# Optimization experiments

Hardware: AMD Instinct MI355X
Metric: run time of the kernel (lower is better)

## Reference

```python
import jax, jax.numpy as jnp
import numpy as np

N = 100000   # nodes
E = 1600000  # edges
H = 2        # heads
F = 64       # out_feats per head
D = 256      # node feature dim
DE = 8       # edge feature dim
NEG_SLOPE = 0.2


def setup_inputs() -> dict:
    key = jax.random.key(0)
    ks = jax.random.split(key, 12)
    s = 0.05
    return {
        "feat_src": jax.random.normal(ks[0], (N, D), jnp.float32),
        "feat_edge": jax.random.normal(ks[1], (E, DE), jnp.float32),
        "edge_src": jax.random.randint(ks[2], (E,), 0, N, jnp.int32),
        "edge_dst": jax.random.randint(ks[3], (E,), 0, N, jnp.int32),
        "W_src": jax.random.normal(ks[4], (H * F, D), jnp.float32) * s,
        "W_dst": jax.random.normal(ks[5], (H * F, D), jnp.float32) * s,
        "b_dst": jax.random.normal(ks[6], (H * F,), jnp.float32) * s,
        "W_attn_src": jax.random.normal(ks[7], (H, D), jnp.float32) * s,
        "W_attn_dst": jax.random.normal(ks[8], (H, D), jnp.float32) * s,
        "W_attn_edge": jax.random.normal(ks[9], (H, DE), jnp.float32) * s,
        "W_ngnn": jax.random.normal(ks[10], (H * F, H * F), jnp.float32) * s,
        "b_ngnn": jax.random.normal(ks[11], (H * F,), jnp.float32) * s,
    }


def reference(feat_src, feat_edge, edge_src, edge_dst,
              W_src, W_dst, b_dst, W_attn_src, W_attn_dst, W_attn_edge,
              W_ngnn, b_ngnn):
    # node projections (graph is not a block -> feat_dst = feat_src)
    h_src = (feat_src @ W_src.T).reshape(N, H, F)          # [N,H,F]
    h_dst = (feat_src @ W_dst.T + b_dst).reshape(N, H, F)  # residual branch

    # per-node attention logits [N,H]
    a_src = feat_src @ W_attn_src.T
    a_dst = feat_src @ W_attn_dst.T
    a_edge = feat_edge @ W_attn_edge.T                     # [E,H]

    # per-edge score: u_add_v + edge term, LeakyReLU
    e = a_src[edge_src] + a_dst[edge_dst] + a_edge         # [E,H]
    e = jnp.where(e >= 0, e, NEG_SLOPE * e)

    # edge softmax over incoming edges of each destination node
    m = jax.ops.segment_max(e, edge_dst, num_segments=N)   # [N,H]
    ex = jnp.exp(e - m[edge_dst])
    z = jax.ops.segment_sum(ex, edge_dst, num_segments=N)  # [N,H]
    a = ex / z[edge_dst]                                   # [E,H]

    # weighted gather-scatter aggregation: u_mul_e -> sum per dst
    msg = h_src[edge_src] * a[:, :, None]                  # [E,H,F]
    rst = jax.ops.segment_sum(msg, edge_dst, num_segments=N)  # [N,H,F]

    # ngnn layer + ReLU
    rst = rst.reshape(N, H * F)
    rst = jax.nn.relu(rst @ W_ngnn.T + b_ngnn)
    rst = rst.reshape(N, H, F)

    # residual connection via dst_fc
    rst = rst + h_dst
    return rst
```

## Files before the change

kernel.cpp:

```cpp
#include <hip/hip_runtime.h>
#include <hip/hip_bf16.h>
#include <math.h>

#define NN 100000
#define EE 1600000
#define DD 256
#define DEE 8
#define HF 128
#define NEG_SLOPE 0.2f
#define NBUCK 196
#define P1_EPB 4096

typedef __bf16 bf16x8 __attribute__((ext_vector_type(8)));
typedef float  f32x4  __attribute__((ext_vector_type(4)));

__device__ inline ushort f2bf(float f) {
    uint32_t x = __builtin_bit_cast(uint32_t, f);
    x += 0x7fffu + ((x >> 16) & 1u);
    return (ushort)(x >> 16);
}
__device__ inline float bf2f(ushort u) {
    uint32_t x = ((uint32_t)u) << 16;
    return __builtin_bit_cast(float, x);
}
__device__ inline float u2f(uint u) { return __builtin_bit_cast(float, u); }
__device__ inline uint f2u(float f) { return __builtin_bit_cast(uint, f); }

__device__ inline void load_lds16(const void* g, void* l) {
    __builtin_amdgcn_global_load_lds(
        (const __attribute__((address_space(1))) void*)g,
        (__attribute__((address_space(3))) void*)l, 16, 0, 0);
}

__global__ __launch_bounds__(256) void f2bf_kernel(
    const float* __restrict__ in, ushort* __restrict__ out, int n)
{
    int i = (blockIdx.x * 256 + threadIdx.x) * 4;
    if (i + 3 < n) {
        float4 v = *(const float4*)(in + i);
        ushort4 o;
        o.x = f2bf(v.x); o.y = f2bf(v.y); o.z = f2bf(v.z); o.w = f2bf(v.w);
        *(ushort4*)(out + i) = o;
    } else {
        for (int c = 0; c < 4 && i + c < n; ++c) out[i + c] = f2bf(in[i + c]);
    }
}

template<int K, int MODE>
__global__ __launch_bounds__(256) void mfma_gemm(
    const ushort* __restrict__ Wb,
    const ushort* __restrict__ Xb,
    const float*  __restrict__ bias,
    const ushort* __restrict__ resid,
    void* __restrict__ outp)
{
    __shared__ ushort As[128 * 32];
    __shared__ ushort Bs[128 * 32];

    const int tid  = threadIdx.x;
    const int lane = tid & 63, wv = tid >> 6;
    const int wm = wv >> 1, wn = wv & 1;
    const int r = lane & 15, quad = lane >> 4;
    const int m0 = blockIdx.x * 128;

    f32x4 acc[4][4] = {};

    for (int k0 = 0; k0 < K; k0 += 32) {
#pragma unroll
        for (int t = 0; t < 2; ++t) {
            int is  = wv + t * 4;
            int row = is * 16 + (lane >> 2);
            int ko  = k0 + (lane & 3) * 8;
            load_lds16(Wb + (size_t)row * K + ko, &As[is * 512]);
            int gm = m0 + row; gm = gm < NN ? gm : NN - 1;
            load_lds16(Xb + (size_t)gm * K + ko, &Bs[is * 512]);
        }
        __syncthreads();
        bf16x8 a[4], b[4];
#pragma unroll
        for (int i = 0; i < 4; ++i) {
            a[i] = __builtin_bit_cast(bf16x8,
                   *(const f32x4*)&As[(wm * 64 + i * 16 + r) * 32 + quad * 8]);
            b[i] = __builtin_bit_cast(bf16x8,
                   *(const f32x4*)&Bs[(wn * 64 + i * 16 + r) * 32 + quad * 8]);
        }
#pragma unroll
        for (int i = 0; i < 4; ++i)
#pragma unroll
            for (int j = 0; j < 4; ++j)
                acc[i][j] = __builtin_amdgcn_mfma_f32_16x16x32_bf16(
                    a[i], b[j], acc[i][j], 0, 0, 0);
        __syncthreads();
    }

#pragma unroll
    for (int i = 0; i < 4; ++i) {
        int fbase = wm * 64 + i * 16 + quad * 4;
        float4 bv = make_float4(0.f, 0.f, 0.f, 0.f);
        if (MODE >= 1) bv = *(const float4*)(bias + fbase);
#pragma unroll
        for (int j = 0; j < 4; ++j) {
            int node = m0 + wn * 64 + j * 16 + r;
            if (node >= NN) continue;
            f32x4 v = acc[i][j];
            if (MODE >= 1) { v[0] += bv.x; v[1] += bv.y; v[2] += bv.z; v[3] += bv.w; }
            if (MODE == 2) {
                ushort4 rs = *(const ushort4*)(resid + (size_t)node * HF + fbase);
                float4 o;
                o.x = fmaxf(v[0], 0.f) + bf2f(rs.x);
                o.y = fmaxf(v[1], 0.f) + bf2f(rs.y);
                o.z = fmaxf(v[2], 0.f) + bf2f(rs.z);
                o.w = fmaxf(v[3], 0.f) + bf2f(rs.w);
                *(float4*)((float*)outp + (size_t)node * HF + fbase) = o;
            } else {
                ushort4 o;
                o.x = f2bf(v[0]); o.y = f2bf(v[1]); o.z = f2bf(v[2]); o.w = f2bf(v[3]);
                *(ushort4*)((ushort*)outp + (size_t)node * HF + fbase) = o;
            }
        }
    }
}

__global__ __launch_bounds__(256) void attn_logits_kernel(
    const float* __restrict__ feat,
    const float* __restrict__ Was, const float* __restrict__ Wad,
    float* __restrict__ a_src, float* __restrict__ a_dst,
    ushort* __restrict__ feat_bf)
{
    int wave = threadIdx.x >> 6, lane = threadIdx.x & 63;
    int node = blockIdx.x * 4 + wave;
    if (node >= NN) return;
    float4 f = *(const float4*)(feat + (size_t)node * DD + lane * 4);
    ushort4 fb;
    fb.x = f2bf(f.x); fb.y = f2bf(f.y); fb.z = f2bf(f.z); fb.w = f2bf(f.w);
    *(ushort4*)(feat_bf + (size_t)node * DD + lane * 4) = fb;

    float4 w0 = *(const float4*)(Was + 0 * DD + lane * 4);
    float4 w1 = *(const float4*)(Was + 1 * DD + lane * 4);
    float4 w2 = *(const float4*)(Wad + 0 * DD + lane * 4);
    float4 w3 = *(const float4*)(Wad + 1 * DD + lane * 4);
    float p0 = f.x * w0.x + f.y * w0.y + f.z * w0.z + f.w * w0.w;
    float p1 = f.x * w1.x + f.y * w1.y + f.z * w1.z + f.w * w1.w;
    float p2 = f.x * w2.x + f.y * w2.y + f.z * w2.z + f.w * w2.w;
    float p3 = f.x * w3.x + f.y * w3.y + f.z * w3.z + f.w * w3.w;
#pragma unroll
    for (int o = 32; o > 0; o >>= 1) {
        p0 += __shfl_xor(p0, o);
        p1 += __shfl_xor(p1, o);
        p2 += __shfl_xor(p2, o);
        p3 += __shfl_xor(p3, o);
    }
    if (lane == 0) {
        a_src[node * 2 + 0] = p0; a_src[node * 2 + 1] = p1;
        a_dst[node * 2 + 0] = p2; a_dst[node * 2 + 1] = p3;
    }
}

__global__ __launch_bounds__(256) void hist_kernel(
    const int* __restrict__ edge_dst, int* __restrict__ deg)
{
    int i = blockIdx.x * 256 + threadIdx.x;
    if (i < EE) atomicAdd(&deg[edge_dst[i]], 1);
}

#define SCAN_ELEMS 1024
__global__ __launch_bounds__(256) void scan1_kernel(
    const int* __restrict__ deg, int* __restrict__ offsets, int* __restrict__ blockSums)
{
    __shared__ int sd[256];
    int tid = threadIdx.x;
    int base = blockIdx.x * SCAN_ELEMS + tid * 4;
    int v[4];
#pragma unroll
    for (int c = 0; c < 4; ++c) v[c] = (base + c < NN) ? deg[base + c] : 0;
    int tsum = v[0] + v[1] + v[2] + v[3];
    sd[tid] = tsum;
    __syncthreads();
    for (int o = 1; o < 256; o <<= 1) {
        int x = (tid >= o) ? sd[tid - o] : 0;
        __syncthreads();
        sd[tid] += x;
        __syncthreads();
    }
    int excl = sd[tid] - tsum;
    int run = excl;
#pragma unroll
    for (int c = 0; c < 4; ++c) {
        if (base + c < NN) offsets[base + c] = run;
        run += v[c];
    }
    if (tid == 255) blockSums[blockIdx.x] = sd[255];
}

__global__ __launch_bounds__(128) void scan2_kernel(int* __restrict__ blockSums, int nb)
{
    __shared__ int sd[128];
    int tid = threadIdx.x;
    int tv = (tid < nb) ? blockSums[tid] : 0;
    sd[tid] = tv;
    __syncthreads();
    for (int o = 1; o < 128; o <<= 1) {
        int x = (tid >= o) ? sd[tid - o] : 0;
        __syncthreads();
        sd[tid] += x;
        __syncthreads();
    }
    if (tid < nb) blockSums[tid] = sd[tid] - tv;
}

__global__ __launch_bounds__(256) void scan3_kernel(
    int* __restrict__ offsets, const int* __restrict__ blockSums)
{
    int tid = threadIdx.x;
    int base = blockIdx.x * SCAN_ELEMS + tid * 4;
    int add = blockSums[blockIdx.x];
#pragma unroll
    for (int c = 0; c < 4; ++c)
        if (base + c < NN) offsets[base + c] += add;
    if (blockIdx.x == 0 && tid == 0) offsets[NN] = EE;
}

__global__ __launch_bounds__(256) void binit_kernel(
    const int* __restrict__ offsets, int* __restrict__ bcur)
{
    int t = threadIdx.x;
    if (t < NBUCK) bcur[t] = offsets[t * 512];
}

__global__ __launch_bounds__(256) void bucket_scatter_kernel(
    const int* __restrict__ edge_src, const int* __restrict__ edge_dst,
    const float* __restrict__ feat_edge,
    const float* __restrict__ a_src, const float* __restrict__ a_dst,
    const float* __restrict__ Wae,
    int* __restrict__ bcur, uint4* __restrict__ staging)
{
    __shared__ int cnt[256];
    __shared__ int basearr[256];
    __shared__ int run[256];
    const int tid = threadIdx.x;
    const int b0 = blockIdx.x * P1_EPB;

    cnt[tid] = 0;
    __syncthreads();
#pragma unroll
    for (int j = 0; j < P1_EPB / 256; ++j) {
        int i = b0 + j * 256 + tid;
        if (i < EE) atomicAdd(&cnt[edge_dst[i] >> 9], 1);
    }
    __syncthreads();
    if (tid < NBUCK) {
        int c = cnt[tid];
        basearr[tid] = c ? atomicAdd(&bcur[tid], c) : 0;
    }
    run[tid] = 0;
    __syncthreads();

    float4 w00 = ((const float4*)Wae)[0], w01 = ((const float4*)Wae)[1];
    float4 w10 = ((const float4*)Wae)[2], w11 = ((const float4*)Wae)[3];

#pragma unroll
    for (int j = 0; j < P1_EPB / 256; ++j) {
        int i = b0 + j * 256 + tid;
        if (i >= EE) continue;
        int s = edge_src[i], d = edge_dst[i];
        float4 e0 = ((const float4*)feat_edge)[i * 2 + 0];
        float4 e1 = ((const float4*)feat_edge)[i * 2 + 1];
        float ae0 = e0.x*w00.x + e0.y*w00.y + e0.z*w00.z + e0.w*w00.w
                  + e1.x*w01.x + e1.y*w01.y + e1.z*w01.z + e1.w*w01.w;
        float ae1 = e0.x*w10.x + e0.y*w10.y + e0.z*w10.z + e0.w*w10.w
                  + e1.x*w11.x + e1.y*w11.y + e1.z*w11.z + e1.w*w11.w;
        float v0 = a_src[s * 2 + 0] + a_dst[d * 2 + 0] + ae0;
        float v1 = a_src[s * 2 + 1] + a_dst[d * 2 + 1] + ae1;
        v0 = (v0 >= 0.f) ? v0 : NEG_SLOPE * v0;
        v1 = (v1 >= 0.f) ? v1 : NEG_SLOPE * v1;
        int bk = d >> 9;
        int ofs = atomicAdd(&run[bk], 1);
        staging[basearr[bk] + ofs] = make_uint4((uint)s, (uint)d, f2u(v0), f2u(v1));
    }
}

__global__ __launch_bounds__(256) void fine_scatter_kernel(
    const int* __restrict__ offsets,
    const uint4* __restrict__ staging, uint4* __restrict__ pairs)
{
    __shared__ int cur[512];
    const int tid = threadIdx.x;
    const int nb0 = blockIdx.x * 512;
    const int ncnt = (NN - nb0 < 512) ? (NN - nb0) : 512;
    for (int i = tid; i < ncnt; i += 256) cur[i] = offsets[nb0 + i];
    __syncthreads();
    const int lo = offsets[nb0];
    const int hi = offsets[nb0 + ncnt];
    for (int j = lo + tid; j < hi; j += 256) {
        uint4 it = staging[j];
        int n = (int)it.y - nb0;
        int pos = atomicAdd(&cur[n], 1);
        pairs[pos] = it;
    }
}

__global__ __launch_bounds__(256) void aggregate_fused(
    const int* __restrict__ offsets,
    const uint4* __restrict__ pairs,
    const ushort* __restrict__ hsrc,
    ushort* __restrict__ agg)
{
    int wave = threadIdx.x >> 6, lane = threadIdx.x & 63;
    int node = blockIdx.x * 4 + wave;
    if (node >= NN) return;
    int off = offsets[node], end = offsets[node + 1];
    int n = end - off;
    uint* aggw = (uint*)agg;
    if (n <= 0) { aggw[(size_t)node * 64 + lane] = 0; return; }
    const uint* h2 = (const uint*)hsrc;
    int hh = lane >> 5;

    float acc0a = 0.f, acc1a = 0.f, acc0b = 0.f, acc1b = 0.f;
    float zi0, zi1;

    if (n <= 64) {
        uint4 pr = (lane < n) ? pairs[off + lane]
                              : make_uint4(0u, 0u, 0xff800000u, 0xff800000u);
        float s0 = u2f(pr.z), s1 = u2f(pr.w);
        float m0 = s0, m1 = s1;
#pragma unroll
        for (int o = 32; o > 0; o >>= 1) {
            m0 = fmaxf(m0, __shfl_xor(m0, o));
            m1 = fmaxf(m1, __shfl_xor(m1, o));
        }
        float ex0 = (lane < n) ? __expf(s0 - m0) : 0.f;
        float ex1 = (lane < n) ? __expf(s1 - m1) : 0.f;
        float z0 = ex0, z1 = ex1;
#pragma unroll
        for (int o = 32; o > 0; o >>= 1) {
            z0 += __shfl_xor(z0, o);
            z1 += __shfl_xor(z1, o);
        }
        zi0 = 1.f / z0; zi1 = 1.f / z1;
        int srcu = (int)pr.x;
        int k = 0;
        for (; k + 1 < n; k += 2) {
            int   sA = __shfl(srcu, k),     sB = __shfl(srcu, k + 1);
            float eA0 = __shfl(ex0, k),     eB0 = __shfl(ex0, k + 1);
            float eA1 = __shfl(ex1, k),     eB1 = __shfl(ex1, k + 1);
            uint pA = h2[(size_t)sA * 64 + lane];
            uint pB = h2[(size_t)sB * 64 + lane];
            float wA = hh ? eA1 : eA0;
            float wB = hh ? eB1 : eB0;
            acc0a = fmaf(wA, bf2f((ushort)(pA & 0xffff)), acc0a);
            acc1a = fmaf(wA, bf2f((ushort)(pA >> 16)),    acc1a);
            acc0b = fmaf(wB, bf2f((ushort)(pB & 0xffff)), acc0b);
            acc1b = fmaf(wB, bf2f((ushort)(pB >> 16)),    acc1b);
        }
        if (k < n) {
            int   sA = __shfl(srcu, k);
            float eA0 = __shfl(ex0, k), eA1 = __shfl(ex1, k);
            uint pA = h2[(size_t)sA * 64 + lane];
            float wA = hh ? eA1 : eA0;
            acc0a = fmaf(wA, bf2f((ushort)(pA & 0xffff)), acc0a);
            acc1a = fmaf(wA, bf2f((ushort)(pA >> 16)),    acc1a);
        }
    } else {
        float m0 = -INFINITY, m1 = -INFINITY;
        for (int c0 = 0; c0 < n; c0 += 64) {
            if (c0 + lane < n) {
                uint4 pr = pairs[off + c0 + lane];
                m0 = fmaxf(m0, u2f(pr.z));
                m1 = fmaxf(m1, u2f(pr.w));
            }
        }
#pragma unroll
        for (int o = 32; o > 0; o >>= 1) {
            m0 = fmaxf(m0, __shfl_xor(m0, o));
            m1 = fmaxf(m1, __shfl_xor(m1, o));
        }
        float z0 = 0.f, z1 = 0.f;
        for (int c0 = 0; c0 < n; c0 += 64) {
            if (c0 + lane < n) {
                uint4 pr = pairs[off + c0 + lane];
                z0 += __expf(u2f(pr.z) - m0);
                z1 += __expf(u2f(pr.w) - m1);
            }
        }
#pragma unroll
        for (int o = 32; o > 0; o >>= 1) {
            z0 += __shfl_xor(z0, o);
            z1 += __shfl_xor(z1, o);
        }
        zi0 = 1.f / z0; zi1 = 1.f / z1;
        for (int c0 = 0; c0 < n; c0 += 64) {
            int cn = n - c0; if (cn > 64) cn = 64;
            uint4 pr = (lane < cn) ? pairs[off + c0 + lane]
                                   : make_uint4(0u, 0u, 0u, 0u);
            float ex0 = (lane < cn) ? __expf(u2f(pr.z) - m0) : 0.f;
            float ex1 = (lane < cn) ? __expf(u2f(pr.w) - m1) : 0.f;
            int srcu = (int)pr.x;
            for (int k = 0; k < cn; ++k) {
                int   sA = __shfl(srcu, k);
                float eA0 = __shfl(ex0, k), eA1 = __shfl(ex1, k);
                uint pA = h2[(size_t)sA * 64 + lane];
                float wA = hh ? eA1 : eA0;
                acc0a = fmaf(wA, bf2f((ushort)(pA & 0xffff)), acc0a);
                acc1a = fmaf(wA, bf2f((ushort)(pA >> 16)),    acc1a);
            }
        }
    }

    float zi = hh ? zi1 : zi0;
    float r0 = (acc0a + acc0b) * zi;
    float r1 = (acc1a + acc1b) * zi;
    aggw[(size_t)node * 64 + lane] = ((uint)f2bf(r1) << 16) | (uint)f2bf(r0);
}

extern "C" void kernel_launch(void* const* d_in, const int* in_sizes, int n_in,
                              void* d_out, int out_size, void* d_ws, size_t ws_size,
                              hipStream_t stream) {
    (void)in_sizes; (void)n_in; (void)out_size; (void)ws_size;
    const float* feat_src  = (const float*)d_in[0];
    const float* feat_edge = (const float*)d_in[1];
    const int*   edge_src  = (const int*)d_in[2];
    const int*   edge_dst  = (const int*)d_in[3];
    const float* W_src     = (const float*)d_in[4];
    const float* W_dst     = (const float*)d_in[5];
    const float* b_dst     = (const float*)d_in[6];
    const float* W_attn_src  = (const float*)d_in[7];
    const float* W_attn_dst  = (const float*)d_in[8];
    const float* W_attn_edge = (const float*)d_in[9];
    const float* W_ngnn    = (const float*)d_in[10];
    const float* b_ngnn    = (const float*)d_in[11];
    float* out = (float*)d_out;

    char* base = (char*)d_ws;
    size_t off = 0;
    auto take = [&](size_t bytes) -> void* {
        void* p = base + off;
        off = (off + bytes + 511) & ~(size_t)511;
        return p;
    };
    ushort* feat_bf  = (ushort*)take((size_t)NN * DD * 2);
    ushort* h_src_bf = (ushort*)take((size_t)NN * HF * 2);
    uint4*  staging  = (uint4*)take((size_t)EE * 16);
    uint4*  pairs    = (uint4*)take((size_t)EE * 16);
    float*  a_src_b  = (float*)take((size_t)NN * 2 * 4);
    float*  a_dst_b  = (float*)take((size_t)NN * 2 * 4);
    int*    deg      = (int*)take((size_t)NN * 4);
    int*    offsets  = (int*)take((size_t)(NN + 1) * 4);
    int*    bcur     = (int*)take((size_t)NBUCK * 4);
    int*    blockSums= (int*)take(512);
    ushort* Wsrc_bf  = (ushort*)take((size_t)HF * DD * 2);
    ushort* Wdst_bf  = (ushort*)take((size_t)HF * DD * 2);
    ushort* Wngnn_bf = (ushort*)take((size_t)HF * HF * 2);
    ushort* h_dst_bf = (ushort*)staging;
    ushort* agg_bf   = feat_bf;

    const int NB_SCAN = (NN + SCAN_ELEMS - 1) / SCAN_ELEMS;
    const int GB_E  = (EE + 255) / 256;
    const int GB_M  = (NN + 127) / 128;
    const int GB_N4 = (NN + 3) / 4;
    const int GB_P1 = (EE + P1_EPB - 1) / P1_EPB;

    hipMemsetAsync(deg, 0, (size_t)NN * 4, stream);
    hipLaunchKernelGGL(hist_kernel, dim3(GB_E), dim3(256), 0, stream, edge_dst, deg);
    hipLaunchKernelGGL(scan1_kernel, dim3(NB_SCAN), dim3(256), 0, stream, deg, offsets, blockSums);
    hipLaunchKernelGGL(scan2_kernel, dim3(1), dim3(128), 0, stream, blockSums, NB_SCAN);
    hipLaunchKernelGGL(scan3_kernel, dim3(NB_SCAN), dim3(256), 0, stream, offsets, blockSums);
    hipLaunchKernelGGL(binit_kernel, dim3(1), dim3(256), 0, stream, offsets, bcur);

    hipLaunchKernelGGL(attn_logits_kernel, dim3(GB_N4), dim3(256), 0, stream,
                       feat_src, W_attn_src, W_attn_dst, a_src_b, a_dst_b, feat_bf);

    hipLaunchKernelGGL(f2bf_kernel, dim3((HF * DD / 4 + 255) / 256), dim3(256), 0, stream,
                       W_src, Wsrc_bf, HF * DD);
    hipLaunchKernelGGL(f2bf_kernel, dim3((HF * DD / 4 + 255) / 256), dim3(256), 0, stream,
                       W_dst, Wdst_bf, HF * DD);
    hipLaunchKernelGGL(f2bf_kernel, dim3((HF * HF / 4 + 255) / 256), dim3(256), 0, stream,
                       W_ngnn, Wngnn_bf, HF * HF);

    hipLaunchKernelGGL(bucket_scatter_kernel, dim3(GB_P1), dim3(256), 0, stream,
                       edge_src, edge_dst, feat_edge, a_src_b, a_dst_b, W_attn_edge,
                       bcur, staging);
    hipLaunchKernelGGL(fine_scatter_kernel, dim3(NBUCK), dim3(256), 0, stream,
                       offsets, staging, pairs);

    hipLaunchKernelGGL((mfma_gemm<DD, 0>), dim3(GB_M), dim3(256), 0, stream,
                       Wsrc_bf, feat_bf, (const float*)nullptr, (const ushort*)nullptr, h_src_bf);
    hipLaunchKernelGGL((mfma_gemm<DD, 1>), dim3(GB_M), dim3(256), 0, stream,
                       Wdst_bf, feat_bf, b_dst, (const ushort*)nullptr, h_dst_bf);

    hipLaunchKernelGGL(aggregate_fused, dim3(GB_N4), dim3(256), 0, stream,
                       offsets, pairs, h_src_bf, agg_bf);

    hipLaunchKernelGGL((mfma_gemm<HF, 2>), dim3(GB_M), dim3(256), 0, stream,
                       Wngnn_bf, agg_bf, b_ngnn, h_dst_bf, out);
}
```

Measured before the change: 550.8 us.

## Fuse src/dst projection GEMMs, merge weight casts, single-pass softmax aggregation

Combines the two node-projection GEMMs into one dual-output kernel that loads each feature tile once, merges the three weight conversion launches into one, and folds the bucket-cursor init into the scan kernel. The aggregation kernel now accumulates the softmax denominator in the same pass as the weighted sum, using an LDS stash instead of shuffles, which removes an extra read of the edge pairs for high-degree nodes. It also shrinks the bucket-scatter block size. Launch count and redundant feature reads go down, at the cost of a smaller node tile in the dual GEMM and more LDS traffic in aggregation.

Result: faster. 521.4 us (-5.3%).

```diff
diff --git a/kernel.cpp b/kernel.cpp
--- a/kernel.cpp
+++ b/kernel.cpp
@@ -9,7 +9,7 @@
 #define HF 128
 #define NEG_SLOPE 0.2f
 #define NBUCK 196
-#define P1_EPB 4096
+#define P1_EPB 1024
 
 typedef __bf16 bf16x8 __attribute__((ext_vector_type(8)));
 typedef float  f32x4  __attribute__((ext_vector_type(4)));
@@ -25,6 +25,8 @@
 }
 __device__ inline float u2f(uint u) { return __builtin_bit_cast(float, u); }
 __device__ inline uint f2u(float f) { return __builtin_bit_cast(uint, f); }
+__device__ inline float lo_bf(uint p) { return __builtin_bit_cast(float, p << 16); }
+__device__ inline float hi_bf(uint p) { return __builtin_bit_cast(float, p & 0xffff0000u); }
 
 __device__ inline void load_lds16(const void* g, void* l) {
     __builtin_amdgcn_global_load_lds(
@@ -32,27 +34,112 @@
         (__attribute__((address_space(3))) void*)l, 16, 0, 0);
 }
 
-__global__ __launch_bounds__(256) void f2bf_kernel(
-    const float* __restrict__ in, ushort* __restrict__ out, int n)
+__global__ __launch_bounds__(256) void f2bf3_kernel(
+    const float* __restrict__ wa, const float* __restrict__ wb,
+    const float* __restrict__ wc,
+    ushort* __restrict__ oa, ushort* __restrict__ ob, ushort* __restrict__ oc)
 {
     int i = (blockIdx.x * 256 + threadIdx.x) * 4;
-    if (i + 3 < n) {
-        float4 v = *(const float4*)(in + i);
-        ushort4 o;
-        o.x = f2bf(v.x); o.y = f2bf(v.y); o.z = f2bf(v.z); o.w = f2bf(v.w);
-        *(ushort4*)(out + i) = o;
-    } else {
-        for (int c = 0; c < 4 && i + c < n; ++c) out[i + c] = f2bf(in[i + c]);
-    }
-}
-
-template<int K, int MODE>
-__global__ __launch_bounds__(256) void mfma_gemm(
+    const int na = HF * DD, nb2 = 2 * HF * DD, nc3 = 2 * HF * DD + HF * HF;
+    const float* src; ushort* dst; int o;
+    if (i < na)       { src = wa; dst = oa; o = i; }
+    else if (i < nb2) { src = wb; dst = ob; o = i - na; }
+    else if (i < nc3) { src = wc; dst = oc; o = i - nb2; }
+    else return;
+    float4 v = *(const float4*)(src + o);
+    ushort4 u;
+    u.x = f2bf(v.x); u.y = f2bf(v.y); u.z = f2bf(v.z); u.w = f2bf(v.w);
+    *(ushort4*)(dst + o) = u;
+}
+
+template<int K>
+__global__ __launch_bounds__(256) void mfma_gemm_dual(
+    const ushort* __restrict__ W0,
+    const ushort* __restrict__ W1,
+    const ushort* __restrict__ Xb,
+    const float*  __restrict__ bias1,
+    ushort* __restrict__ out0, ushort* __restrict__ out1)
+{
+    __shared__ ushort As[2][128 * 32];
+    __shared__ ushort Bs[64 * 32];
+
+    const int tid  = threadIdx.x;
+    const int lane = tid & 63, wv = tid >> 6;
+    const int wm = wv >> 1, wn = wv & 1;
+    const int r = lane & 15, quad = lane >> 4;
+    const int m0 = blockIdx.x * 64;
+
+    f32x4 acc[2][4][2] = {};
+
+    for (int k0 = 0; k0 < K; k0 += 32) {
+#pragma unroll
+        for (int t = 0; t < 2; ++t) {
+            int is  = wv + t * 4;
+            int row = is * 16 + (lane >> 2);
+            int ko  = k0 + (lane & 3) * 8;
+            load_lds16(W0 + (size_t)row * K + ko, &As[0][is * 512]);
+            load_lds16(W1 + (size_t)row * K + ko, &As[1][is * 512]);
+        }
+        {
+            int is  = wv;
+            int row = is * 16 + (lane >> 2);
+            int ko  = k0 + (lane & 3) * 8;
+            int gm = m0 + row; gm = gm < NN ? gm : NN - 1;
+            load_lds16(Xb + (size_t)gm * K + ko, &Bs[is * 512]);
+        }
+        __syncthreads();
+        bf16x8 a[2][4], b[2];
+#pragma unroll
+        for (int i = 0; i < 4; ++i) {
+            a[0][i] = __builtin_bit_cast(bf16x8,
+                      *(const f32x4*)&As[0][(wm * 64 + i * 16 + r) * 32 + quad * 8]);
+            a[1][i] = __builtin_bit_cast(bf16x8,
+                      *(const f32x4*)&As[1][(wm * 64 + i * 16 + r) * 32 + quad * 8]);
+        }
+#pragma unroll
+        for (int j = 0; j < 2; ++j)
+            b[j] = __builtin_bit_cast(bf16x8,
+                   *(const f32x4*)&Bs[(wn * 32 + j * 16 + r) * 32 + quad * 8]);
+#pragma unroll
+        for (int s = 0; s < 2; ++s)
+#pragma unroll
+            for (int i = 0; i < 4; ++i)
+#pragma unroll
+                for (int j = 0; j < 2; ++j)
+                    acc[s][i][j] = __builtin_amdgcn_mfma_f32_16x16x32_bf16(
+                        a[s][i], b[j], acc[s][i][j], 0, 0, 0);
+        __syncthreads();
+    }
+
+#pragma unroll
+    for (int s = 0; s < 2; ++s) {
+        ushort* outp = s ? out1 : out0;
+#pragma unroll
+        for (int i = 0; i < 4; ++i) {
+            int fbase = wm * 64 + i * 16 + quad * 4;
+            float4 bv = make_float4(0.f, 0.f, 0.f, 0.f);
+            if (s == 1) bv = *(const float4*)(bias1 + fbase);
+#pragma unroll
+            for (int j = 0; j < 2; ++j) {
+                int node = m0 + wn * 32 + j * 16 + r;
+                if (node >= NN) continue;
+                f32x4 v = acc[s][i][j];
+                v[0] += bv.x; v[1] += bv.y; v[2] += bv.z; v[3] += bv.w;
+                ushort4 o;
+                o.x = f2bf(v[0]); o.y = f2bf(v[1]); o.z = f2bf(v[2]); o.w = f2bf(v[3]);
+                *(ushort4*)(outp + (size_t)node * HF + fbase) = o;
+            }
+        }
+    }
+}
+
+template<int K>
+__global__ __launch_bounds__(256) void mfma_gemm_ngnn(
     const ushort* __restrict__ Wb,
     const ushort* __restrict__ Xb,
     const float*  __restrict__ bias,
     const ushort* __restrict__ resid,
-    void* __restrict__ outp)
+    float* __restrict__ outp)
 {
     __shared__ ushort As[128 * 32];
     __shared__ ushort Bs[128 * 32];
@@ -96,27 +183,19 @@
 #pragma unroll
     for (int i = 0; i < 4; ++i) {
         int fbase = wm * 64 + i * 16 + quad * 4;
-        float4 bv = make_float4(0.f, 0.f, 0.f, 0.f);
-        if (MODE >= 1) bv = *(const float4*)(bias + fbase);
+        float4 bv = *(const float4*)(bias + fbase);
 #pragma unroll
         for (int j = 0; j < 4; ++j) {
             int node = m0 + wn * 64 + j * 16 + r;
             if (node >= NN) continue;
             f32x4 v = acc[i][j];
-            if (MODE >= 1) { v[0] += bv.x; v[1] += bv.y; v[2] += bv.z; v[3] += bv.w; }
-            if (MODE == 2) {
-                ushort4 rs = *(const ushort4*)(resid + (size_t)node * HF + fbase);
-                float4 o;
-                o.x = fmaxf(v[0], 0.f) + bf2f(rs.x);
-                o.y = fmaxf(v[1], 0.f) + bf2f(rs.y);
-                o.z = fmaxf(v[2], 0.f) + bf2f(rs.z);
-                o.w = fmaxf(v[3], 0.f) + bf2f(rs.w);
-                *(float4*)((float*)outp + (size_t)node * HF + fbase) = o;
-            } else {
-                ushort4 o;
-                o.x = f2bf(v[0]); o.y = f2bf(v[1]); o.z = f2bf(v[2]); o.w = f2bf(v[3]);
-                *(ushort4*)((ushort*)outp + (size_t)node * HF + fbase) = o;
-            }
+            ushort4 rs = *(const ushort4*)(resid + (size_t)node * HF + fbase);
+            float4 o;
+            o.x = fmaxf(v[0] + bv.x, 0.f) + bf2f(rs.x);
+            o.y = fmaxf(v[1] + bv.y, 0.f) + bf2f(rs.y);
+            o.z = fmaxf(v[2] + bv.z, 0.f) + bf2f(rs.z);
+            o.w = fmaxf(v[3] + bv.w, 0.f) + bf2f(rs.w);
+            *(float4*)(outp + (size_t)node * HF + fbase) = o;
         }
     }
 }
@@ -209,22 +288,22 @@
 }
 
 __global__ __launch_bounds__(256) void scan3_kernel(
-    int* __restrict__ offsets, const int* __restrict__ blockSums)
+    int* __restrict__ offsets, const int* __restrict__ blockSums,
+    int* __restrict__ bcur)
 {
     int tid = threadIdx.x;
     int base = blockIdx.x * SCAN_ELEMS + tid * 4;
     int add = blockSums[blockIdx.x];
 #pragma unroll
-    for (int c = 0; c < 4; ++c)
-        if (base + c < NN) offsets[base + c] += add;
+    for (int c = 0; c < 4; ++c) {
+        int idx = base + c;
+        if (idx < NN) {
+            int v = offsets[idx] + add;
+            offsets[idx] = v;
+            if ((idx & 511) == 0) bcur[idx >> 9] = v;
+        }
+    }
     if (blockIdx.x == 0 && tid == 0) offsets[NN] = EE;
-}
-
-__global__ __launch_bounds__(256) void binit_kernel(
-    const int* __restrict__ offsets, int* __restrict__ bcur)
-{
-    int t = threadIdx.x;
-    if (t < NBUCK) bcur[t] = offsets[t * 512];
 }
 
 __global__ __launch_bounds__(256) void bucket_scatter_kernel(
@@ -305,6 +384,7 @@
     const ushort* __restrict__ hsrc,
     ushort* __restrict__ agg)
 {
+    __shared__ uint4 stash[4][64];
     int wave = threadIdx.x >> 6, lane = threadIdx.x & 63;
     int node = blockIdx.x * 4 + wave;
     if (node >= NN) return;
@@ -315,50 +395,29 @@
     const uint* h2 = (const uint*)hsrc;
     int hh = lane >> 5;
 
-    float acc0a = 0.f, acc1a = 0.f, acc0b = 0.f, acc1b = 0.f;
-    float zi0, zi1;
+    float acc0 = 0.f, acc1 = 0.f, z0 = 0.f, z1 = 0.f;
 
     if (n <= 64) {
         uint4 pr = (lane < n) ? pairs[off + lane]
                               : make_uint4(0u, 0u, 0xff800000u, 0xff800000u);
-        float s0 = u2f(pr.z), s1 = u2f(pr.w);
-        float m0 = s0, m1 = s1;
+        float m0 = u2f(pr.z), m1 = u2f(pr.w);
 #pragma unroll
         for (int o = 32; o > 0; o >>= 1) {
             m0 = fmaxf(m0, __shfl_xor(m0, o));
             m1 = fmaxf(m1, __shfl_xor(m1, o));
         }
-        float ex0 = (lane < n) ? __expf(s0 - m0) : 0.f;
-        float ex1 = (lane < n) ? __expf(s1 - m1) : 0.f;
-        float z0 = ex0, z1 = ex1;
-#pragma unroll
-        for (int o = 32; o > 0; o >>= 1) {
-            z0 += __shfl_xor(z0, o);
-            z1 += __shfl_xor(z1, o);
-        }
-        zi0 = 1.f / z0; zi1 = 1.f / z1;
-        int srcu = (int)pr.x;
-        int k = 0;
-        for (; k + 1 < n; k += 2) {
-            int   sA = __shfl(srcu, k),     sB = __shfl(srcu, k + 1);
-            float eA0 = __shfl(ex0, k),     eB0 = __shfl(ex0, k + 1);
-            float eA1 = __shfl(ex1, k),     eB1 = __shfl(ex1, k + 1);
-            uint pA = h2[(size_t)sA * 64 + lane];
-            uint pB = h2[(size_t)sB * 64 + lane];
-            float wA = hh ? eA1 : eA0;
-            float wB = hh ? eB1 : eB0;
-            acc0a = fmaf(wA, bf2f((ushort)(pA & 0xffff)), acc0a);
-            acc1a = fmaf(wA, bf2f((ushort)(pA >> 16)),    acc1a);
-            acc0b = fmaf(wB, bf2f((ushort)(pB & 0xffff)), acc0b);
-            acc1b = fmaf(wB, bf2f((ushort)(pB >> 16)),    acc1b);
-        }
-        if (k < n) {
-            int   sA = __shfl(srcu, k);
-            float eA0 = __shfl(ex0, k), eA1 = __shfl(ex1, k);
-            uint pA = h2[(size_t)sA * 64 + lane];
-            float wA = hh ? eA1 : eA0;
-            acc0a = fmaf(wA, bf2f((ushort)(pA & 0xffff)), acc0a);
-            acc1a = fmaf(wA, bf2f((ushort)(pA >> 16)),    acc1a);
+        float ex0 = (lane < n) ? __expf(u2f(pr.z) - m0) : 0.f;
+        float ex1 = (lane < n) ? __expf(u2f(pr.w) - m1) : 0.f;
+        z0 = ex0; z1 = ex1;
+        stash[wave][lane] = make_uint4(pr.x, f2u(ex0), f2u(ex1), 0u);
+        __builtin_amdgcn_wave_barrier();
+#pragma unroll 4
+        for (int k = 0; k < n; ++k) {
+            uint4 st = stash[wave][k];
+            uint p = h2[(size_t)st.x * 64 + lane];
+            float w = hh ? u2f(st.z) : u2f(st.y);
+            acc0 = fmaf(w, lo_bf(p), acc0);
+            acc1 = fmaf(w, hi_bf(p), acc1);
         }
     } else {
         float m0 = -INFINITY, m1 = -INFINITY;
@@ -374,41 +433,39 @@
             m0 = fmaxf(m0, __shfl_xor(m0, o));
             m1 = fmaxf(m1, __shfl_xor(m1, o));
         }
-        float z0 = 0.f, z1 = 0.f;
-        for (int c0 = 0; c0 < n; c0 += 64) {
-            if (c0 + lane < n) {
-                uint4 pr = pairs[off + c0 + lane];
-                z0 += __expf(u2f(pr.z) - m0);
-                z1 += __expf(u2f(pr.w) - m1);
-            }
-        }
-#pragma unroll
-        for (int o = 32; o > 0; o >>= 1) {
-            z0 += __shfl_xor(z0, o);
-            z1 += __shfl_xor(z1, o);
-        }
-        zi0 = 1.f / z0; zi1 = 1.f / z1;
         for (int c0 = 0; c0 < n; c0 += 64) {
             int cn = n - c0; if (cn > 64) cn = 64;
-            uint4 pr = (lane < cn) ? pairs[off + c0 + lane]
-                                   : make_uint4(0u, 0u, 0u, 0u);
-            float ex0 = (lane < cn) ? __expf(u2f(pr.z) - m0) : 0.f;
-            float ex1 = (lane < cn) ? __expf(u2f(pr.w) - m1) : 0.f;
-            int srcu = (int)pr.x;
+            uint srcv = 0; float ex0 = 0.f, ex1 = 0.f;
+            if (lane < cn) {
+                uint4 pr = pairs[off + c0 + lane];
+                srcv = pr.x;
+                ex0 = __expf(u2f(pr.z) - m0);
+                ex1 = __expf(u2f(pr.w) - m1);
+                z0 += ex0; z1 += ex1;
+            }
+            stash[wave][lane] = make_uint4(srcv, f2u(ex0), f2u(ex1), 0u);
+            __builtin_amdgcn_wave_barrier();
+#pragma unroll 4
             for (int k = 0; k < cn; ++k) {
-                int   sA = __shfl(srcu, k);
-                float eA0 = __shfl(ex0, k), eA1 = __shfl(ex1, k);
-                uint pA = h2[(size_t)sA * 64 + lane];
-                float wA = hh ? eA1 : eA0;
-                acc0a = fmaf(wA, bf2f((ushort)(pA & 0xffff)), acc0a);
-                acc1a = fmaf(wA, bf2f((ushort)(pA >> 16)),    acc1a);
+                uint4 st = stash[wave][k];
+                uint p = h2[(size_t)st.x * 64 + lane];
+                float w = hh ? u2f(st.z) : u2f(st.y);
+                acc0 = fmaf(w, lo_bf(p), acc0);
+                acc1 = fmaf(w, hi_bf(p), acc1);
             }
-        }
-    }
-
-    float zi = hh ? zi1 : zi0;
-    float r0 = (acc0a + acc0b) * zi;
-    float r1 = (acc1a + acc1b) * zi;
+            __builtin_amdgcn_wave_barrier();
+        }
+    }
+
+#pragma unroll
+    for (int o = 32; o > 0; o >>= 1) {
+        z0 += __shfl_xor(z0, o);
+        z1 += __shfl_xor(z1, o);
+    }
+    float zi = hh ? ((z1 > 0.f) ? 1.f / z1 : 0.f)
+                  : ((z0 > 0.f) ? 1.f / z0 : 0.f);
+    float r0 = acc0 * zi;
+    float r1 = acc1 * zi;
     aggw[(size_t)node * 64 + lane] = ((uint)f2bf(r1) << 16) | (uint)f2bf(r0);
 }
 
@@ -456,25 +513,23 @@
     const int NB_SCAN = (NN + SCAN_ELEMS - 1) / SCAN_ELEMS;
     const int GB_E  = (EE + 255) / 256;
     const int GB_M  = (NN + 127) / 128;
+    const int GB_M64= (NN + 63) / 64;
     const int GB_N4 = (NN + 3) / 4;
     const int GB_P1 = (EE + P1_EPB - 1) / P1_EPB;
+    const int W3_N  = (2 * HF * DD + HF * HF) / 4;
+    const int GB_W3 = (W3_N + 255) / 256;
 
     hipMemsetAsync(deg, 0, (size_t)NN * 4, stream);
     hipLaunchKernelGGL(hist_kernel, dim3(GB_E), dim3(256), 0, stream, edge_dst, deg);
     hipLaunchKernelGGL(scan1_kernel, dim3(NB_SCAN), dim3(256), 0, stream, deg, offsets, blockSums);
     hipLaunchKernelGGL(scan2_kernel, dim3(1), dim3(128), 0, stream, blockSums, NB_SCAN);
-    hipLaunchKernelGGL(scan3_kernel, dim3(NB_SCAN), dim3(256), 0, stream, offsets, blockSums);
-    hipLaunchKernelGGL(binit_kernel, dim3(1), dim3(256), 0, stream, offsets, bcur);
+    hipLaunchKernelGGL(scan3_kernel, dim3(NB_SCAN), dim3(256), 0, stream, offsets, blockSums, bcur);
 
     hipLaunchKernelGGL(attn_logits_kernel, dim3(GB_N4), dim3(256), 0, stream,
                        feat_src, W_attn_src, W_attn_dst, a_src_b, a_dst_b, feat_bf);
 
-    hipLaunchKernelGGL(f2bf_kernel, dim3((HF * DD / 4 + 255) / 256), dim3(256), 0, stream,
-                       W_src, Wsrc_bf, HF * DD);
-    hipLaunchKernelGGL(f2bf_kernel, dim3((HF * DD / 4 + 255) / 256), dim3(256), 0, stream,
-                       W_dst, Wdst_bf, HF * DD);
-    hipLaunchKernelGGL(f2bf_kernel, dim3((HF * HF / 4 + 255) / 256), dim3(256), 0, stream,
-                       W_ngnn, Wngnn_bf, HF * HF);
+    hipLaunchKernelGGL(f2bf3_kernel, dim3(GB_W3), dim3(256), 0, stream,
+                       W_src, W_dst, W_ngnn, Wsrc_bf, Wdst_bf, Wngnn_bf);
 
     hipLaunchKernelGGL(bucket_scatter_kernel, dim3(GB_P1), dim3(256), 0, stream,
                        edge_src, edge_dst, feat_edge, a_src_b, a_dst_b, W_attn_edge,
@@ -482,14 +537,12 @@
     hipLaunchKernelGGL(fine_scatter_kernel, dim3(NBUCK), dim3(256), 0, stream,
                        offsets, staging, pairs);
 
-    hipLaunchKernelGGL((mfma_gemm<DD, 0>), dim3(GB_M), dim3(256), 0, stream,
-                       Wsrc_bf, feat_bf, (const float*)nullptr, (const ushort*)nullptr, h_src_bf);
-    hipLaunchKernelGGL((mfma_gemm<DD, 1>), dim3(GB_M), dim3(256), 0, stream,
-                       Wdst_bf, feat_bf, b_dst, (const ushort*)nullptr, h_dst_bf);
+    hipLaunchKernelGGL((mfma_gemm_dual<DD>), dim3(GB_M64), dim3(256), 0, stream,
+                       Wsrc_bf, Wdst_bf, feat_bf, b_dst, h_src_bf, h_dst_bf);
 
     hipLaunchKernelGGL(aggregate_fused, dim3(GB_N4), dim3(256), 0, stream,
                        offsets, pairs, h_src_bf, agg_bf);
 
-    hipLaunchKernelGGL((mfma_gemm<HF, 2>), dim3(GB_M), dim3(256), 0, stream,
+    hipLaunchKernelGGL((mfma_gemm_ngnn<HF>), dim3(GB_M), dim3(256), 0, stream,
                        Wngnn_bf, agg_bf, b_ngnn, h_dst_bf, out);
 }
```
